# Performance work log

Hardware: AMD Instinct MI355X
Metric: run time of the kernel (lower is better)

Reference implementation:

```python
import jax, jax.numpy as jnp
import numpy as np

# Model dims
P_SPECS = [(6, 256), (7, 256)]          # pattern_length -> num_patterns (ordered)
P = 512                                  # total_num_patterns
MAXL = 7                                 # max_pattern_length
ND = 2                                   # num_diags (self-loop diag + main diag)
D = 300                                  # embedding_dim
V = 50000                                # vocab size
B = 32                                   # batch size
T = 128                                  # max_doc_len
NC = 2                                   # num_classes
NEG = -1e30                              # max-sum semiring zero; one = 0.0
END_STATES = np.concatenate([np.full(n, l - 1, dtype=np.int32) for l, n in P_SPECS])


def setup_inputs() -> dict:
    key = jax.random.key(0)
    ks = jax.random.split(key, 8)
    tokens = jax.random.randint(ks[0], (B, T), 0, V, dtype=jnp.int32)
    doc_lens = jax.random.randint(ks[1], (B,), 64, T + 1, dtype=jnp.int32)
    emb_table = jax.random.normal(ks[2], (V, D), dtype=jnp.float32)
    diags = jax.random.normal(ks[3], (P * ND * MAXL, D), dtype=jnp.float32)
    diags = diags / jnp.linalg.norm(diags, axis=1, keepdims=True)  # normalize(diags)
    bias = jax.random.normal(ks[4], (P * ND * MAXL, 1), dtype=jnp.float32)
    epsilons = jax.random.normal(ks[5], (P, MAXL - 1), dtype=jnp.float32)
    bn_weight = jnp.ones((P,), jnp.float32)
    bn_bias = jnp.zeros((P,), jnp.float32)
    final_w = 0.05 * jax.random.normal(ks[6], (NC, P), dtype=jnp.float32)
    final_b = jnp.zeros((NC,), jnp.float32)
    return dict(tokens=tokens, doc_lens=doc_lens, emb_table=emb_table, diags=diags,
                bias=bias, epsilons=epsilons, bn_weight=bn_weight, bn_bias=bn_bias,
                final_w=final_w, final_b=final_b)


def reference(tokens, doc_lens, emb_table, diags, bias, epsilons,
              bn_weight, bn_bias, final_w, final_b):
    # --- transition matrices (max-sum semiring: from_outer is identity) ---
    emb = emb_table[tokens]                                   # [B,T,D]
    # mm(diags, embeddings) + bias_scale * bias  (bias_scale = 1.0)
    ts = jnp.einsum('btd,kd->btk', emb, diags) + bias[:, 0]   # [B,T,P*ND*MAXL]
    ts = ts.reshape(B, T, P, ND, MAXL)                        # [B,T,P,ND,MAXL]

    end = jnp.asarray(END_STATES)                             # [P]
    hid0 = jnp.full((B, P, MAXL), NEG, jnp.float32).at[:, :, 0].set(0.0)
    sc0 = jnp.full((B, P), NEG, jnp.float32)                  # semiring.zero
    zpad = jnp.full((B, P, 1), NEG, jnp.float32)              # zero_padding
    rpad = jnp.zeros((B, P, 1), jnp.float32)                  # restart_padding (one)

    # epsilon_values = epsilon_scale (one=0) + epsilons
    def step(carry, xs):
        hid, sc = carry
        tm, i = xs                                            # tm: [B,P,ND,MAXL]
        # epsilon transitions
        ae = jnp.maximum(hid, jnp.concatenate([zpad, hid[:, :, :-1] + epsilons], axis=2))
        # main path: diag index -1 (the main diagonal)
        main = jnp.concatenate([rpad, ae[:, :, :-1] + tm[:, :, -1, :-1]], axis=2)
        # self loops: diag 0, self_loop_scale = semiring.one = 0
        sl = ae + tm[:, :, 0, :]
        hid = jnp.maximum(main, sl)
        endv = jnp.take_along_axis(hid, jnp.broadcast_to(end[None, :, None], (B, P, 1)), axis=2)[:, :, 0]
        sc = jnp.where((doc_lens > i)[:, None], jnp.maximum(sc, endv), sc)
        return (hid, sc), None

    (_, scores), _ = jax.lax.scan(step, (hid0, sc0),
                                  (jnp.moveaxis(ts, 1, 0), jnp.arange(T, dtype=jnp.int32)))

    # BatchNorm1d (training mode: biased batch statistics)
    mean = scores.mean(axis=0)
    var = scores.var(axis=0)
    scores = (scores - mean) * jax.lax.rsqrt(var + 1e-5) * bn_weight + bn_bias
    # binarize_scores
    scores = jnp.sign(jax.nn.relu(scores))
    # final linear layer
    return scores @ final_w.T + final_b                       # [B, NC]
```

## Files before the change

### kernel.cpp

```cpp
#include <hip/hip_runtime.h>

#define BB 32
#define TT 128
#define PP 512
#define DD 300
#define KT 10
#define NX 7168
#define AT 256
#define BT 448
#define NEG -1e30f

typedef _Float16 half8 __attribute__((ext_vector_type(8)));
typedef float floatx4 __attribute__((ext_vector_type(4)));

__device__ __forceinline__ void async_load16(const void* g, void* l) {
    __builtin_amdgcn_global_load_lds(
        (const __attribute__((address_space(1))) void*)g,
        (__attribute__((address_space(3))) void*)l, 16, 0, 0);
}

__device__ __forceinline__ floatx4 mfma16(half8 a, half8 b, floatx4 c) {
    return __builtin_amdgcn_mfma_f32_16x16x32_f16(a, b, c, 0, 0, 0);
}

__global__ __launch_bounds__(256) void pack_kernel(
    const int* __restrict__ tokens, const float* __restrict__ emb,
    const float* __restrict__ diags, const float* __restrict__ bias,
    _Float16* __restrict__ AhP, _Float16* __restrict__ AlP,
    _Float16* __restrict__ BhP, _Float16* __restrict__ BlP)
{
    const int idx = blockIdx.x * 256 + threadIdx.x;
    if (idx >= (AT + BT) * KT * 64) return;
    const int chunk = idx >> 6;
    const int ln = idx & 63;

    const float* src;
    float kslot;
    _Float16 *dh, *dl;
    int kt;
    if (chunk < AT * KT) {
        const int mt = chunk / KT; kt = chunk - mt * KT;
        const int m = mt * 16 + (ln & 15);
        src = emb + (size_t)tokens[m] * DD;
        kslot = 1.0f;
        dh = AhP + (size_t)chunk * 512 + ln * 8;
        dl = AlP + (size_t)chunk * 512 + ln * 8;
    } else {
        const int c2 = chunk - AT * KT;
        const int nt = c2 / KT; kt = c2 - nt * KT;
        const int n = nt * 16 + (ln & 15);
        src = diags + (size_t)n * DD;
        kslot = bias[n];
        dh = BhP + (size_t)c2 * 512 + ln * 8;
        dl = BlP + (size_t)c2 * 512 + ln * 8;
    }

    const int k0 = kt * 32 + (ln >> 4) * 8;
    float v[8];
    if (k0 + 8 <= DD) {
        float4 a = *(const float4*)(src + k0);
        float4 b = *(const float4*)(src + k0 + 4);
        v[0] = a.x; v[1] = a.y; v[2] = a.z; v[3] = a.w;
        v[4] = b.x; v[5] = b.y; v[6] = b.z; v[7] = b.w;
    } else {
        #pragma unroll
        for (int i = 0; i < 8; ++i) {
            const int k = k0 + i;
            v[i] = (k < DD) ? src[k] : (k == DD ? kslot : 0.f);
        }
    }
    half8 h, l;
    #pragma unroll
    for (int i = 0; i < 8; ++i) {
        h[i] = (_Float16)v[i];
        l[i] = (_Float16)((v[i] - (float)h[i]) * 4096.f);
    }
    *(half8*)dh = h;
    *(half8*)dl = l;
}

__global__ __launch_bounds__(256, 2) void gemm_kernel(
    const _Float16* __restrict__ AhP, const _Float16* __restrict__ AlP,
    const _Float16* __restrict__ BhP, const _Float16* __restrict__ BlP,
    float* __restrict__ C)
{
    __shared__ __align__(16) _Float16 Bs[2][2][8][512];

    const int tid = threadIdx.x;
    const int w = tid >> 6, ln = tid & 63;
    const int n0t = blockIdx.x * 8, m0t = blockIdx.y * 8;
    const int wm = w & 1, wn = w >> 1;

    floatx4 acc0[4][4], acc1[4][4];
    #pragma unroll
    for (int i = 0; i < 4; ++i)
        #pragma unroll
        for (int j = 0; j < 4; ++j) {
            acc0[i][j] = (floatx4){0.f, 0.f, 0.f, 0.f};
            acc1[i][j] = (floatx4){0.f, 0.f, 0.f, 0.f};
        }

    half8 ah[2][4], al[2][4];

    auto loadA = [&](int kt, int pb) {
        #pragma unroll
        for (int i = 0; i < 4; ++i) {
            const size_t ch = ((size_t)(m0t + wm * 4 + i) * KT + kt) * 512 + ln * 8;
            ah[pb][i] = *(const half8*)(AhP + ch);
            al[pb][i] = *(const half8*)(AlP + ch);
        }
    };
    auto stageB = [&](int kt, int buf) {
        #pragma unroll
        for (int s = 0; s < 2; ++s) {
            const int nt = w + s * 4;
            const size_t ch = ((size_t)(n0t + nt) * KT + kt) * 512 + ln * 8;
            async_load16(BhP + ch, &Bs[buf][0][nt][0]);
            async_load16(BlP + ch, &Bs[buf][1][nt][0]);
        }
    };

    stageB(0, 0);
    loadA(0, 0);
    __syncthreads();

    #pragma unroll
    for (int kt = 0; kt < KT; ++kt) {
        const int cb = kt & 1, nb = cb ^ 1;
        if (kt + 1 < KT) {
            loadA(kt + 1, nb);
            stageB(kt + 1, nb);
        }
        #pragma unroll
        for (int j = 0; j < 4; ++j) {
            const half8 bh = *(const half8*)&Bs[cb][0][wn * 4 + j][ln * 8];
            const half8 bl = *(const half8*)&Bs[cb][1][wn * 4 + j][ln * 8];
            #pragma unroll
            for (int i = 0; i < 4; ++i) {
                acc0[i][j] = mfma16(ah[cb][i], bh, acc0[i][j]);
                acc1[i][j] = mfma16(ah[cb][i], bl, acc1[i][j]);
                acc1[i][j] = mfma16(al[cb][i], bh, acc1[i][j]);
            }
        }
        __syncthreads();
    }

    #pragma unroll
    for (int j = 0; j < 4; ++j) {
        const int n = (n0t + wn * 4 + j) * 16 + (ln & 15);
        #pragma unroll
        for (int i = 0; i < 4; ++i) {
            const int mb = (m0t + wm * 4 + i) * 16 + (ln >> 4) * 4;
            #pragma unroll
            for (int r = 0; r < 4; ++r)
                C[(size_t)(mb + r) * NX + n] =
                    acc0[i][j][r] + acc1[i][j][r] * (1.0f / 4096.0f);
        }
    }
}

__global__ __launch_bounds__(64) void scan_kernel(
    const float* __restrict__ ts,
    const float* __restrict__ epsilons,
    const int* __restrict__ doc_lens,
    float* __restrict__ scores)
{
    const int b = blockIdx.x;
    const int p = blockIdx.y * 64 + threadIdx.x;
    const int dl = doc_lens[b];

    float e[6];
    #pragma unroll
    for (int i = 0; i < 6; ++i) e[i] = epsilons[p * 6 + i];

    const float* base = ts + (size_t)b * TT * NX + p * 14;

    float h0 = 0.f, h1 = NEG, h2 = NEG, h3 = NEG, h4 = NEG, h5 = NEG, h6 = NEG;
    float sc = NEG;
    const bool end5 = (p < 256);

    float2 buf[4][7];

    auto load = [&](int slot, int t) {
        const float2* s = (const float2*)(base + (size_t)t * NX);
        #pragma unroll
        for (int i = 0; i < 7; ++i) buf[slot][i] = s[i];
    };
    auto step = [&](int slot) {
        const float2* v = buf[slot];
        float ae0 = h0;
        float ae1 = fmaxf(h1, h0 + e[0]);
        float ae2 = fmaxf(h2, h1 + e[1]);
        float ae3 = fmaxf(h3, h2 + e[2]);
        float ae4 = fmaxf(h4, h3 + e[3]);
        float ae5 = fmaxf(h5, h4 + e[4]);
        float ae6 = fmaxf(h6, h5 + e[5]);
        h0 = fmaxf(0.f,            ae0 + v[0].x);
        h1 = fmaxf(ae0 + v[3].y,   ae1 + v[0].y);
        h2 = fmaxf(ae1 + v[4].x,   ae2 + v[1].x);
        h3 = fmaxf(ae2 + v[4].y,   ae3 + v[1].y);
        h4 = fmaxf(ae3 + v[5].x,   ae4 + v[2].x);
        h5 = fmaxf(ae4 + v[5].y,   ae5 + v[2].y);
        h6 = fmaxf(ae5 + v[6].x,   ae6 + v[3].x);
        sc = fmaxf(sc, end5 ? h5 : h6);
    };

    #pragma unroll
    for (int j = 0; j < 4; ++j) load(j, j);

    int tb = 0;
    for (; tb + 4 <= dl; tb += 4) {
        #pragma unroll
        for (int j = 0; j < 4; ++j) {
            step(j);
            load(j, tb + j + 4);
        }
    }
    const int rem = dl - tb;
    #pragma unroll
    for (int j = 0; j < 3; ++j)
        if (j < rem) step(j);

    scores[p * BB + b] = sc;
}

__global__ __launch_bounds__(512) void finalize_kernel(
    const float* __restrict__ scores,
    const float* __restrict__ bn_w,
    const float* __restrict__ bn_b,
    const float* __restrict__ fw,
    const float* __restrict__ fb,
    float* __restrict__ out)
{
    __shared__ float acc[64];
    const int p = threadIdx.x;
    if (p < 64) acc[p] = 0.f;
    __syncthreads();

    float x[32];
    const float4* sp = (const float4*)(scores + p * 32);
    #pragma unroll
    for (int i = 0; i < 8; ++i) ((float4*)x)[i] = sp[i];

    float mean = 0.f;
    #pragma unroll
    for (int i = 0; i < 32; ++i) mean += x[i];
    mean *= (1.f / 32.f);
    float var = 0.f;
    #pragma unroll
    for (int i = 0; i < 32; ++i) { const float d = x[i] - mean; var = fmaf(d, d, var); }
    var *= (1.f / 32.f);

    const float scale = (1.f / sqrtf(var + 1e-5f)) * bn_w[p];
    const float shift = bn_b[p];
    const float w0 = fw[p], w1 = fw[PP + p];

    for (int b = 0; b < 32; ++b) {
        const float v = (x[b] - mean) * scale + shift;
        const bool bin = v > 0.f;
        float v0 = bin ? w0 : 0.f;
        float v1 = bin ? w1 : 0.f;
        #pragma unroll
        for (int o = 32; o; o >>= 1) {
            v0 += __shfl_xor(v0, o);
            v1 += __shfl_xor(v1, o);
        }
        if ((threadIdx.x & 63) == 0) {
            atomicAdd(&acc[b * 2 + 0], v0);
            atomicAdd(&acc[b * 2 + 1], v1);
        }
    }
    __syncthreads();
    if (p < 64) out[p] = acc[p] + fb[p & 1];
}

extern "C" void kernel_launch(void* const* d_in, const int* in_sizes, int n_in,
                              void* d_out, int out_size, void* d_ws, size_t ws_size,
                              hipStream_t stream) {
    const int*   tokens   = (const int*)d_in[0];
    const int*   doc_lens = (const int*)d_in[1];
    const float* emb      = (const float*)d_in[2];
    const float* diags    = (const float*)d_in[3];
    const float* bias     = (const float*)d_in[4];
    const float* eps      = (const float*)d_in[5];
    const float* bnw      = (const float*)d_in[6];
    const float* bnb      = (const float*)d_in[7];
    const float* fw       = (const float*)d_in[8];
    const float* fb       = (const float*)d_in[9];
    float* out = (float*)d_out;

    float* ts     = (float*)d_ws;
    float* scores = ts + (size_t)4096 * NX;
    _Float16* AhP = (_Float16*)(scores + PP * BB);
    _Float16* AlP = AhP + (size_t)AT * KT * 512;
    _Float16* BhP = AlP + (size_t)AT * KT * 512;
    _Float16* BlP = BhP + (size_t)BT * KT * 512;

    pack_kernel<<<(AT + BT) * KT * 64 / 256, 256, 0, stream>>>(
        tokens, emb, diags, bias, AhP, AlP, BhP, BlP);
    gemm_kernel<<<dim3(BT / 8, AT / 8), 256, 0, stream>>>(AhP, AlP, BhP, BlP, ts);
    scan_kernel<<<dim3(BB, PP / 64), 64, 0, stream>>>(ts, eps, doc_lens, scores);
    finalize_kernel<<<1, 512, 0, stream>>>(scores, bnw, bnb, fw, fb, out);
}
```

Baseline: 202.7 us.

## Skip GEMM tiles past doc length and triple-buffer B staging with manual waits

```diff
diff --git a/kernel.cpp b/kernel.cpp
--- a/kernel.cpp
+++ b/kernel.cpp
@@ -82,15 +82,20 @@
 __global__ __launch_bounds__(256, 2) void gemm_kernel(
     const _Float16* __restrict__ AhP, const _Float16* __restrict__ AlP,
     const _Float16* __restrict__ BhP, const _Float16* __restrict__ BlP,
+    const int* __restrict__ doc_lens,
     float* __restrict__ C)
 {
-    __shared__ __align__(16) _Float16 Bs[2][2][8][512];
+    __shared__ __align__(16) _Float16 Bs[3][2][8][512];
 
     const int tid = threadIdx.x;
     const int w = tid >> 6, ln = tid & 63;
     const int n0t = blockIdx.x * 8, m0t = blockIdx.y * 8;
     const int wm = w & 1, wn = w >> 1;
 
+    const int dl = doc_lens[blockIdx.y];
+    const int nlive = (dl + 15) >> 4;
+    const int ilim = (nlive - wm + 1) >> 1;
+
     floatx4 acc0[4][4], acc1[4][4];
     #pragma unroll
     for (int i = 0; i < 4; ++i)
@@ -105,7 +110,7 @@
     auto loadA = [&](int kt, int pb) {
         #pragma unroll
         for (int i = 0; i < 4; ++i) {
-            const size_t ch = ((size_t)(m0t + wm * 4 + i) * KT + kt) * 512 + ln * 8;
+            const size_t ch = ((size_t)(m0t + wm + 2 * i) * KT + kt) * 512 + ln * 8;
             ah[pb][i] = *(const half8*)(AhP + ch);
             al[pb][i] = *(const half8*)(AlP + ch);
         }
@@ -122,27 +127,40 @@
 
     stageB(0, 0);
     loadA(0, 0);
-    __syncthreads();
+    stageB(1, 1);
 
     #pragma unroll
     for (int kt = 0; kt < KT; ++kt) {
-        const int cb = kt & 1, nb = cb ^ 1;
-        if (kt + 1 < KT) {
-            loadA(kt + 1, nb);
-            stageB(kt + 1, nb);
-        }
+        const int lb = kt % 3, ar = kt & 1;
+        if (kt + 2 < KT) stageB(kt + 2, (kt + 2) % 3);
+        if (kt + 1 < KT) loadA(kt + 1, ar ^ 1);
+
+        if (kt < 2)       asm volatile("s_waitcnt vmcnt(24)" ::: "memory");
+        else if (kt < 8)  asm volatile("s_waitcnt vmcnt(32)" ::: "memory");
+        else if (kt == 8) asm volatile("s_waitcnt vmcnt(28)" ::: "memory");
+        else              asm volatile("s_waitcnt vmcnt(16)" ::: "memory");
+        __builtin_amdgcn_sched_barrier(0);
+        __builtin_amdgcn_s_barrier();
+        __builtin_amdgcn_sched_barrier(0);
+
+        __builtin_amdgcn_s_setprio(1);
         #pragma unroll
         for (int j = 0; j < 4; ++j) {
-            const half8 bh = *(const half8*)&Bs[cb][0][wn * 4 + j][ln * 8];
-            const half8 bl = *(const half8*)&Bs[cb][1][wn * 4 + j][ln * 8];
+            const half8 bh = *(const half8*)&Bs[lb][0][wn * 4 + j][ln * 8];
+            const half8 bl = *(const half8*)&Bs[lb][1][wn * 4 + j][ln * 8];
             #pragma unroll
             for (int i = 0; i < 4; ++i) {
-                acc0[i][j] = mfma16(ah[cb][i], bh, acc0[i][j]);
-                acc1[i][j] = mfma16(ah[cb][i], bl, acc1[i][j]);
-                acc1[i][j] = mfma16(al[cb][i], bh, acc1[i][j]);
+                if (i < ilim) {
+                    acc0[i][j] = mfma16(ah[ar][i], bh, acc0[i][j]);
+                    acc1[i][j] = mfma16(ah[ar][i], bl, acc1[i][j]);
+                    acc1[i][j] = mfma16(al[ar][i], bh, acc1[i][j]);
+                }
             }
         }
-        __syncthreads();
+        __builtin_amdgcn_s_setprio(0);
+        __builtin_amdgcn_sched_barrier(0);
+        if (kt + 1 < KT) __builtin_amdgcn_s_barrier();
+        __builtin_amdgcn_sched_barrier(0);
     }
 
     #pragma unroll
@@ -150,11 +168,13 @@
         const int n = (n0t + wn * 4 + j) * 16 + (ln & 15);
         #pragma unroll
         for (int i = 0; i < 4; ++i) {
-            const int mb = (m0t + wm * 4 + i) * 16 + (ln >> 4) * 4;
-            #pragma unroll
-            for (int r = 0; r < 4; ++r)
-                C[(size_t)(mb + r) * NX + n] =
-                    acc0[i][j][r] + acc1[i][j][r] * (1.0f / 4096.0f);
+            if (i < ilim) {
+                const int mb = (m0t + wm + 2 * i) * 16 + (ln >> 4) * 4;
+                #pragma unroll
+                for (int r = 0; r < 4; ++r)
+                    C[(size_t)(mb + r) * NX + n] =
+                        acc0[i][j][r] + acc1[i][j][r] * (1.0f / 4096.0f);
+            }
         }
     }
 }
@@ -298,7 +318,8 @@
 
     pack_kernel<<<(AT + BT) * KT * 64 / 256, 256, 0, stream>>>(
         tokens, emb, diags, bias, AhP, AlP, BhP, BlP);
-    gemm_kernel<<<dim3(BT / 8, AT / 8), 256, 0, stream>>>(AhP, AlP, BhP, BlP, ts);
+    gemm_kernel<<<dim3(BT / 8, AT / 8), 256, 0, stream>>>(
+        AhP, AlP, BhP, BlP, doc_lens, ts);
     scan_kernel<<<dim3(BB, PP / 64), 64, 0, stream>>>(ts, eps, doc_lens, scores);
     finalize_kernel<<<1, 512, 0, stream>>>(scores, bnw, bnb, fw, fb, out);
 }
```

Measured after the change: 201.4 us. About the same (-0.6%).

## Fuse GEMM with recurrence scan, keeping transition scores in shared memory

Applied to the files above, without the earlier changes.

```diff
diff --git a/kernel.cpp b/kernel.cpp
--- a/kernel.cpp
+++ b/kernel.cpp
@@ -5,9 +5,9 @@
 #define PP 512
 #define DD 300
 #define KT 10
-#define NX 7168
 #define AT 256
 #define BT 448
+#define CTS 114
 #define NEG -1e30f
 
 typedef _Float16 half8 __attribute__((ext_vector_type(8)));
@@ -79,44 +79,51 @@
     *(half8*)dl = l;
 }
 
-__global__ __launch_bounds__(256, 2) void gemm_kernel(
+__global__ __launch_bounds__(256, 2) void gemm_scan_kernel(
     const _Float16* __restrict__ AhP, const _Float16* __restrict__ AlP,
     const _Float16* __restrict__ BhP, const _Float16* __restrict__ BlP,
-    float* __restrict__ C)
+    const float* __restrict__ epsilons,
+    const int* __restrict__ doc_lens,
+    float* __restrict__ scores)
 {
-    __shared__ __align__(16) _Float16 Bs[2][2][8][512];
+    __shared__ __align__(16) unsigned char smem[128 * CTS * 4];
+    typedef _Float16 BsT[2][7][512];
+    BsT* Bs = reinterpret_cast<BsT*>(smem);
+    float (*Ct)[CTS] = reinterpret_cast<float(*)[CTS]>(smem);
 
     const int tid = threadIdx.x;
     const int w = tid >> 6, ln = tid & 63;
-    const int n0t = blockIdx.x * 8, m0t = blockIdx.y * 8;
-    const int wm = w & 1, wn = w >> 1;
-
-    floatx4 acc0[4][4], acc1[4][4];
-    #pragma unroll
-    for (int i = 0; i < 4; ++i)
-        #pragma unroll
-        for (int j = 0; j < 4; ++j) {
+    const int bx = blockIdx.x;
+    const int b  = blockIdx.y;
+
+    floatx4 acc0[2][7], acc1[2][7];
+    #pragma unroll
+    for (int i = 0; i < 2; ++i)
+        #pragma unroll
+        for (int j = 0; j < 7; ++j) {
             acc0[i][j] = (floatx4){0.f, 0.f, 0.f, 0.f};
             acc1[i][j] = (floatx4){0.f, 0.f, 0.f, 0.f};
         }
 
-    half8 ah[2][4], al[2][4];
+    half8 ah[2][2], al[2][2];
 
     auto loadA = [&](int kt, int pb) {
         #pragma unroll
-        for (int i = 0; i < 4; ++i) {
-            const size_t ch = ((size_t)(m0t + wm * 4 + i) * KT + kt) * 512 + ln * 8;
+        for (int i = 0; i < 2; ++i) {
+            const size_t ch = ((size_t)(b * 8 + 2 * w + i) * KT + kt) * 512 + ln * 8;
             ah[pb][i] = *(const half8*)(AhP + ch);
             al[pb][i] = *(const half8*)(AlP + ch);
         }
     };
     auto stageB = [&](int kt, int buf) {
         #pragma unroll
-        for (int s = 0; s < 2; ++s) {
-            const int nt = w + s * 4;
-            const size_t ch = ((size_t)(n0t + nt) * KT + kt) * 512 + ln * 8;
-            async_load16(BhP + ch, &Bs[buf][0][nt][0]);
-            async_load16(BlP + ch, &Bs[buf][1][nt][0]);
+        for (int s = 0; s < 4; ++s) {
+            const int cidx = w + 4 * s;
+            if (cidx < 14) {
+                const int nt = cidx >> 1, hl = cidx & 1;
+                const size_t ch = ((size_t)(7 * bx + nt) * KT + kt) * 512 + ln * 8;
+                async_load16((hl ? BlP : BhP) + ch, &Bs[buf][hl][nt][0]);
+            }
         }
     };
 
@@ -132,11 +139,11 @@
             stageB(kt + 1, nb);
         }
         #pragma unroll
-        for (int j = 0; j < 4; ++j) {
-            const half8 bh = *(const half8*)&Bs[cb][0][wn * 4 + j][ln * 8];
-            const half8 bl = *(const half8*)&Bs[cb][1][wn * 4 + j][ln * 8];
+        for (int j = 0; j < 7; ++j) {
+            const half8 bh = *(const half8*)&Bs[cb][0][j][ln * 8];
+            const half8 bl = *(const half8*)&Bs[cb][1][j][ln * 8];
             #pragma unroll
-            for (int i = 0; i < 4; ++i) {
+            for (int i = 0; i < 2; ++i) {
                 acc0[i][j] = mfma16(ah[cb][i], bh, acc0[i][j]);
                 acc1[i][j] = mfma16(ah[cb][i], bl, acc1[i][j]);
                 acc1[i][j] = mfma16(al[cb][i], bh, acc1[i][j]);
@@ -146,48 +153,39 @@
     }
 
     #pragma unroll
-    for (int j = 0; j < 4; ++j) {
-        const int n = (n0t + wn * 4 + j) * 16 + (ln & 15);
-        #pragma unroll
-        for (int i = 0; i < 4; ++i) {
-            const int mb = (m0t + wm * 4 + i) * 16 + (ln >> 4) * 4;
+    for (int j = 0; j < 7; ++j) {
+        const int col = j * 16 + (ln & 15);
+        #pragma unroll
+        for (int i = 0; i < 2; ++i) {
+            const int rb = (2 * w + i) * 16 + (ln >> 4) * 4;
             #pragma unroll
             for (int r = 0; r < 4; ++r)
-                C[(size_t)(mb + r) * NX + n] =
-                    acc0[i][j][r] + acc1[i][j][r] * (1.0f / 4096.0f);
-        }
-    }
-}
-
-__global__ __launch_bounds__(64) void scan_kernel(
-    const float* __restrict__ ts,
-    const float* __restrict__ epsilons,
-    const int* __restrict__ doc_lens,
-    float* __restrict__ scores)
-{
-    const int b = blockIdx.x;
-    const int p = blockIdx.y * 64 + threadIdx.x;
+                Ct[rb + r][col] = acc0[i][j][r] + acc1[i][j][r] * (1.0f / 4096.0f);
+        }
+    }
+    __syncthreads();
+    if (w != 0) return;
+    if (ln >= 8) return;
+
+    const int p = bx * 8 + ln;
     const int dl = doc_lens[b];
+    const int c0 = ln * 14;
+    const bool end5 = (p < 256);
 
     float e[6];
     #pragma unroll
     for (int i = 0; i < 6; ++i) e[i] = epsilons[p * 6 + i];
-
-    const float* base = ts + (size_t)b * TT * NX + p * 14;
 
     float h0 = 0.f, h1 = NEG, h2 = NEG, h3 = NEG, h4 = NEG, h5 = NEG, h6 = NEG;
     float sc = NEG;
-    const bool end5 = (p < 256);
-
-    float2 buf[4][7];
-
-    auto load = [&](int slot, int t) {
-        const float2* s = (const float2*)(base + (size_t)t * NX);
-        #pragma unroll
-        for (int i = 0; i < 7; ++i) buf[slot][i] = s[i];
-    };
-    auto step = [&](int slot) {
-        const float2* v = buf[slot];
+
+    float2 fa[7], fb[7];
+    auto ldrow = [&](int t, float2* f) {
+        const float* row = &Ct[t][c0];
+        #pragma unroll
+        for (int i = 0; i < 7; ++i) f[i] = *(const float2*)(row + 2 * i);
+    };
+    auto stepv = [&](const float2* v) {
         float ae0 = h0;
         float ae1 = fmaxf(h1, h0 + e[0]);
         float ae2 = fmaxf(h2, h1 + e[1]);
@@ -195,31 +193,25 @@
         float ae4 = fmaxf(h4, h3 + e[3]);
         float ae5 = fmaxf(h5, h4 + e[4]);
         float ae6 = fmaxf(h6, h5 + e[5]);
-        h0 = fmaxf(0.f,            ae0 + v[0].x);
-        h1 = fmaxf(ae0 + v[3].y,   ae1 + v[0].y);
-        h2 = fmaxf(ae1 + v[4].x,   ae2 + v[1].x);
-        h3 = fmaxf(ae2 + v[4].y,   ae3 + v[1].y);
-        h4 = fmaxf(ae3 + v[5].x,   ae4 + v[2].x);
-        h5 = fmaxf(ae4 + v[5].y,   ae5 + v[2].y);
-        h6 = fmaxf(ae5 + v[6].x,   ae6 + v[3].x);
+        h0 = fmaxf(0.f,          ae0 + v[0].x);
+        h1 = fmaxf(ae0 + v[3].y, ae1 + v[0].y);
+        h2 = fmaxf(ae1 + v[4].x, ae2 + v[1].x);
+        h3 = fmaxf(ae2 + v[4].y, ae3 + v[1].y);
+        h4 = fmaxf(ae3 + v[5].x, ae4 + v[2].x);
+        h5 = fmaxf(ae4 + v[5].y, ae5 + v[2].y);
+        h6 = fmaxf(ae5 + v[6].x, ae6 + v[3].x);
         sc = fmaxf(sc, end5 ? h5 : h6);
     };
 
-    #pragma unroll
-    for (int j = 0; j < 4; ++j) load(j, j);
-
-    int tb = 0;
-    for (; tb + 4 <= dl; tb += 4) {
-        #pragma unroll
-        for (int j = 0; j < 4; ++j) {
-            step(j);
-            load(j, tb + j + 4);
-        }
-    }
-    const int rem = dl - tb;
-    #pragma unroll
-    for (int j = 0; j < 3; ++j)
-        if (j < rem) step(j);
+    ldrow(0, fa);
+    int t = 0;
+    for (; t + 2 <= dl; t += 2) {
+        ldrow(t + 1, fb);
+        stepv(fa);
+        ldrow(t + 2 <= 127 ? t + 2 : 127, fa);
+        stepv(fb);
+    }
+    if (t < dl) stepv(fa);
 
     scores[p * BB + b] = sc;
 }
@@ -289,8 +281,7 @@
     const float* fb       = (const float*)d_in[9];
     float* out = (float*)d_out;
 
-    float* ts     = (float*)d_ws;
-    float* scores = ts + (size_t)4096 * NX;
+    float* scores = (float*)d_ws;
     _Float16* AhP = (_Float16*)(scores + PP * BB);
     _Float16* AlP = AhP + (size_t)AT * KT * 512;
     _Float16* BhP = AlP + (size_t)AT * KT * 512;
@@ -298,7 +289,7 @@
 
     pack_kernel<<<(AT + BT) * KT * 64 / 256, 256, 0, stream>>>(
         tokens, emb, diags, bias, AhP, AlP, BhP, BlP);
-    gemm_kernel<<<dim3(BT / 8, AT / 8), 256, 0, stream>>>(AhP, AlP, BhP, BlP, ts);
-    scan_kernel<<<dim3(BB, PP / 64), 64, 0, stream>>>(ts, eps, doc_lens, scores);
+    gemm_scan_kernel<<<dim3(64, BB), 256, 0, stream>>>(
+        AhP, AlP, BhP, BlP, eps, doc_lens, scores);
     finalize_kernel<<<1, 512, 0, stream>>>(scores, bnw, bnb, fw, fb, out);
 }
```

Result: slower. 216.2 us (+6.6%).

## Load B fragments directly from global memory and skip stores past doc length

Applied to the files above, without the earlier changes.

```diff
diff --git a/kernel.cpp b/kernel.cpp
--- a/kernel.cpp
+++ b/kernel.cpp
@@ -12,12 +12,6 @@
 
 typedef _Float16 half8 __attribute__((ext_vector_type(8)));
 typedef float floatx4 __attribute__((ext_vector_type(4)));
-
-__device__ __forceinline__ void async_load16(const void* g, void* l) {
-    __builtin_amdgcn_global_load_lds(
-        (const __attribute__((address_space(1))) void*)g,
-        (__attribute__((address_space(3))) void*)l, 16, 0, 0);
-}
 
 __device__ __forceinline__ floatx4 mfma16(half8 a, half8 b, floatx4 c) {
     return __builtin_amdgcn_mfma_f32_16x16x32_f16(a, b, c, 0, 0, 0);
@@ -82,15 +76,16 @@
 __global__ __launch_bounds__(256, 2) void gemm_kernel(
     const _Float16* __restrict__ AhP, const _Float16* __restrict__ AlP,
     const _Float16* __restrict__ BhP, const _Float16* __restrict__ BlP,
+    const int* __restrict__ doc_lens,
     float* __restrict__ C)
 {
-    __shared__ __align__(16) _Float16 Bs[2][2][8][512];
-
     const int tid = threadIdx.x;
     const int w = tid >> 6, ln = tid & 63;
     const int n0t = blockIdx.x * 8, m0t = blockIdx.y * 8;
     const int wm = w & 1, wn = w >> 1;
 
+    const int dl = doc_lens[blockIdx.y];
+
     floatx4 acc0[4][4], acc1[4][4];
     #pragma unroll
     for (int i = 0; i < 4; ++i)
@@ -110,31 +105,18 @@
             al[pb][i] = *(const half8*)(AlP + ch);
         }
     };
-    auto stageB = [&](int kt, int buf) {
-        #pragma unroll
-        for (int s = 0; s < 2; ++s) {
-            const int nt = w + s * 4;
-            const size_t ch = ((size_t)(n0t + nt) * KT + kt) * 512 + ln * 8;
-            async_load16(BhP + ch, &Bs[buf][0][nt][0]);
-            async_load16(BlP + ch, &Bs[buf][1][nt][0]);
-        }
-    };
-
-    stageB(0, 0);
+
     loadA(0, 0);
-    __syncthreads();
 
     #pragma unroll
     for (int kt = 0; kt < KT; ++kt) {
         const int cb = kt & 1, nb = cb ^ 1;
-        if (kt + 1 < KT) {
-            loadA(kt + 1, nb);
-            stageB(kt + 1, nb);
-        }
+        if (kt + 1 < KT) loadA(kt + 1, nb);
         #pragma unroll
         for (int j = 0; j < 4; ++j) {
-            const half8 bh = *(const half8*)&Bs[cb][0][wn * 4 + j][ln * 8];
-            const half8 bl = *(const half8*)&Bs[cb][1][wn * 4 + j][ln * 8];
+            const size_t ch = ((size_t)(n0t + wn * 4 + j) * KT + kt) * 512 + ln * 8;
+            const half8 bh = *(const half8*)(BhP + ch);
+            const half8 bl = *(const half8*)(BlP + ch);
             #pragma unroll
             for (int i = 0; i < 4; ++i) {
                 acc0[i][j] = mfma16(ah[cb][i], bh, acc0[i][j]);
@@ -142,7 +124,6 @@
                 acc1[i][j] = mfma16(al[cb][i], bh, acc1[i][j]);
             }
         }
-        __syncthreads();
     }
 
     #pragma unroll
@@ -150,11 +131,13 @@
         const int n = (n0t + wn * 4 + j) * 16 + (ln & 15);
         #pragma unroll
         for (int i = 0; i < 4; ++i) {
-            const int mb = (m0t + wm * 4 + i) * 16 + (ln >> 4) * 4;
-            #pragma unroll
-            for (int r = 0; r < 4; ++r)
-                C[(size_t)(mb + r) * NX + n] =
-                    acc0[i][j][r] + acc1[i][j][r] * (1.0f / 4096.0f);
+            if ((wm * 4 + i) * 16 < dl) {
+                const int mb = (m0t + wm * 4 + i) * 16 + (ln >> 4) * 4;
+                #pragma unroll
+                for (int r = 0; r < 4; ++r)
+                    C[(size_t)(mb + r) * NX + n] =
+                        acc0[i][j][r] + acc1[i][j][r] * (1.0f / 4096.0f);
+            }
         }
     }
 }
@@ -213,7 +196,8 @@
         #pragma unroll
         for (int j = 0; j < 4; ++j) {
             step(j);
-            load(j, tb + j + 4);
+            const int t = tb + j + 4;
+            load(j, t > 127 ? 127 : t);
         }
     }
     const int rem = dl - tb;
@@ -298,7 +282,8 @@
 
     pack_kernel<<<(AT + BT) * KT * 64 / 256, 256, 0, stream>>>(
         tokens, emb, diags, bias, AhP, AlP, BhP, BlP);
-    gemm_kernel<<<dim3(BT / 8, AT / 8), 256, 0, stream>>>(AhP, AlP, BhP, BlP, ts);
+    gemm_kernel<<<dim3(BT / 8, AT / 8), 256, 0, stream>>>(
+        AhP, AlP, BhP, BlP, doc_lens, ts);
     scan_kernel<<<dim3(BB, PP / 64), 64, 0, stream>>>(ts, eps, doc_lens, scores);
     finalize_kernel<<<1, 512, 0, stream>>>(scores, bnw, bnb, fw, fb, out);
 }
```

Result: slower. 237.9 us (+17.3%).
